# Optimization experiments

Hardware: AMD Instinct MI355X
Metric: run time of the kernel (lower is better)

The kernel has to match this reference:

```python
import jax, jax.numpy as jnp
import numpy as np
from jax import lax

M, N, Q = 256, 65536, 64
LAMBDA_STAR = 0.1
LAMBDA_O = 0.1
T_ITERS = 16
PM_ITERS = 100


def setup_inputs() -> dict:
    key = jax.random.key(0)
    kx, kd = jax.random.split(key)
    X = jax.random.normal(kx, (M, N), dtype=jnp.float32)
    D = jax.random.normal(kd, (M, Q), dtype=jnp.float32)
    return {"X": X, "D": D}


def _power_method(D):
    # Largest eigenvalue of D^T D via 100-step power iteration (fixed random init).
    x0 = jax.random.normal(jax.random.key(1), (1, Q), dtype=D.dtype)

    def step(x, _):
        x = (x @ D.T) @ D          # [1,q] -> [1,m] -> [1,q]
        nm = jnp.linalg.norm(x)
        return x / nm, nm

    _, nms = lax.scan(step, x0, None, length=PM_ITERS)
    return nms[-1]


def reference(X, D):
    m, n = X.shape
    q = D.shape[1]
    alpha = _power_method(D)
    eta = 1.0 / alpha

    Iq = jnp.eye(q, dtype=D.dtype)
    Im = jnp.eye(m, dtype=D.dtype)
    top = jnp.concatenate([D.T @ D + LAMBDA_STAR * Iq, D.T], axis=1)   # [q, q+m]
    bot = jnp.concatenate([D, (1.0 + LAMBDA_STAR) * Im], axis=1)       # [m, q+m]
    H = jnp.eye(m + q, dtype=D.dtype) - eta * jnp.concatenate([top, bot], axis=0)
    W = eta * jnp.concatenate([D.T, Im], axis=0)                        # [(m+q), m]
    t = LAMBDA_O * eta * jnp.concatenate([jnp.zeros(q, D.dtype), jnp.ones(m, D.dtype)])

    b0 = W @ X                                                           # [(m+q), n]
    Z0 = jnp.zeros((m + q, n), dtype=X.dtype)

    def ista_step(carry, _):
        Z, b = carry
        Znew = jnp.maximum(0.0, b - t[:, None])    # thresholding (ger(t, ones) == t broadcast)
        b = b + H @ (Znew - Z)
        return (Znew, b), None

    (Z, _), _ = lax.scan(ista_step, (Z0, b0), None, length=T_ITERS)
    return Z
```

## Files before the change

kernel.cpp:

```cpp
#include <hip/hip_runtime.h>


typedef __bf16 bf16x8 __attribute__((ext_vector_type(8)));
typedef __bf16 bf16x2 __attribute__((ext_vector_type(2)));
typedef float f32x4 __attribute__((ext_vector_type(4)));
typedef float f32x2 __attribute__((ext_vector_type(2)));

#define MFMA16(a, b, c) __builtin_amdgcn_mfma_f32_16x16x32_bf16((a), (b), (c), 0, 0, 0)

#define NTOT 65536
#define NCOL 16

__device__ __forceinline__ unsigned pk2(float a, float b) {
#if __has_builtin(__builtin_amdgcn_cvt_pk_bf16_f32)
  return __builtin_bit_cast(unsigned, __builtin_amdgcn_cvt_pk_bf16_f32(a, b));
#else
  unsigned short ua = __builtin_bit_cast(unsigned short, (__bf16)a);
  unsigned short ub = __builtin_bit_cast(unsigned short, (__bf16)b);
  return (unsigned)ua | ((unsigned)ub << 16);
#endif
}
__device__ __forceinline__ unsigned pk2v(f32x2 v) { return pk2(v[0], v[1]); }
__device__ __forceinline__ f32x2 f2(float s) { f32x2 v = {s, s}; return v; }
__device__ __forceinline__ f32x2 pfma(f32x2 a, f32x2 b, f32x2 c) {
  return __builtin_elementwise_fma(a, b, c);
}
__device__ __forceinline__ f32x2 pmax0(f32x2 a) {
  return __builtin_elementwise_max(a, f2(0.f));
}

#define GOF(row) ((row) * 68 + (((row) >> 3) << 2))
__global__ void rnmf_prep(const float* __restrict__ D, void* __restrict__ ws) {
  float* wsf = (float*)ws;
  __bf16* Dbf = (__bf16*)((char*)ws + 256);
  __bf16* DTbf = (__bf16*)((char*)ws + 256 + 32768);

  __shared__ __bf16 DTl[64 * 264];
  __shared__ __bf16 gA[64 * 72];
  __shared__ __bf16 gB[64 * 72];
  __shared__ float gf[64 * 68 + 32];
  __shared__ __align__(16) float xv[64];

  const int tid = threadIdx.x;
  const int w = tid >> 6, lane = tid & 63, c = lane & 15, q4 = lane >> 4;

#pragma unroll
  for (int e = 0; e < 16; ++e) {
    int i4 = e * 256 + tid;
    float4 dv = *(const float4*)(D + i4 * 4);
    uint2 u; u.x = pk2(dv.x, dv.y); u.y = pk2(dv.z, dv.w);
    *(uint2*)(Dbf + i4 * 4) = u;
  }
#pragma unroll
  for (int e = 0; e < 64; ++e) {
    int flat = e * 256 + tid;
    int k = flat >> 6, a = flat & 63;
    DTl[a * 264 + k] = (__bf16)D[k * 64 + a];
  }
  __syncthreads();
#pragma unroll
  for (int e = 0; e < 8; ++e) {
    int fi = e * 256 + tid;
    int a = fi >> 5;
    int k = (fi * 8) & 255;
    *(bf16x8*)(DTbf + fi * 8) = *(const bf16x8*)&DTl[a * 264 + k];
  }
#pragma unroll
  for (int ct = 0; ct < 4; ++ct) {
    f32x4 acc = {0.f, 0.f, 0.f, 0.f};
#pragma unroll
    for (int kb = 0; kb < 8; ++kb) {
      bf16x8 a = *(const bf16x8*)&DTl[(16 * w + c) * 264 + 32 * kb + 8 * q4];
      bf16x8 b = *(const bf16x8*)&DTl[(16 * ct + c) * 264 + 32 * kb + 8 * q4];
      acc = MFMA16(a, b, acc);
    }
#pragma unroll
    for (int r = 0; r < 4; ++r)
      gA[(16 * w + 4 * q4 + r) * 72 + 16 * ct + c] = (__bf16)acc[r];
  }
  __syncthreads();
#pragma unroll
  for (int ct = 0; ct < 4; ++ct) {
    f32x4 acc = {0.f, 0.f, 0.f, 0.f};
#pragma unroll
    for (int kb = 0; kb < 2; ++kb) {
      bf16x8 a = *(const bf16x8*)&gA[(16 * w + c) * 72 + 32 * kb + 8 * q4];
      bf16x8 b = *(const bf16x8*)&gA[(16 * ct + c) * 72 + 32 * kb + 8 * q4];
      acc = MFMA16(a, b, acc);
    }
#pragma unroll
    for (int r = 0; r < 4; ++r)
      gB[(16 * w + 4 * q4 + r) * 72 + 16 * ct + c] = (__bf16)acc[r];
  }
  __syncthreads();
#pragma unroll
  for (int ct = 0; ct < 4; ++ct) {
    f32x4 acc = {0.f, 0.f, 0.f, 0.f};
#pragma unroll
    for (int kb = 0; kb < 2; ++kb) {
      bf16x8 a = *(const bf16x8*)&gB[(16 * w + c) * 72 + 32 * kb + 8 * q4];
      bf16x8 b = *(const bf16x8*)&gB[(16 * ct + c) * 72 + 32 * kb + 8 * q4];
      acc = MFMA16(a, b, acc);
    }
#pragma unroll
    for (int r = 0; r < 4; ++r)
      gA[(16 * w + 4 * q4 + r) * 72 + 16 * ct + c] = (__bf16)acc[r];
  }
  __syncthreads();
#pragma unroll
  for (int ct = 0; ct < 4; ++ct) {
    f32x4 acc = {0.f, 0.f, 0.f, 0.f};
#pragma unroll
    for (int kb = 0; kb < 2; ++kb) {
      bf16x8 a = *(const bf16x8*)&gA[(16 * w + c) * 72 + 32 * kb + 8 * q4];
      bf16x8 b = *(const bf16x8*)&gA[(16 * ct + c) * 72 + 32 * kb + 8 * q4];
      acc = MFMA16(a, b, acc);
    }
#pragma unroll
    for (int r = 0; r < 4; ++r)
      gf[GOF(16 * w + 4 * q4 + r) + 16 * ct + c] = acc[r];
  }
  __syncthreads();

  if (w == 0) {
    float td = gf[GOF(lane) + lane];
#pragma unroll
    for (int off = 32; off; off >>= 1) td += __shfl_xor(td, off, 64);
    const float tr = td;
    const float itr = 1.f / tr;
    xv[lane] = 1.f;
    float nm = 1.f;
    const int rowoff = GOF(lane);
    for (int itp = 0; itp < 28; ++itp) {
      float a0 = 0.f, a1 = 0.f, a2 = 0.f, a3 = 0.f;
#pragma unroll
      for (int k = 0; k < 64; k += 16) {
        float4 ga = *(const float4*)&gf[rowoff + k];
        float4 xa = *(const float4*)&xv[k];
        float4 gb = *(const float4*)&gf[rowoff + k + 4];
        float4 xb = *(const float4*)&xv[k + 4];
        float4 gc = *(const float4*)&gf[rowoff + k + 8];
        float4 xc = *(const float4*)&xv[k + 8];
        float4 gd = *(const float4*)&gf[rowoff + k + 12];
        float4 xd = *(const float4*)&xv[k + 12];
        a0 = fmaf(ga.x, xa.x, a0); a0 = fmaf(ga.y, xa.y, a0);
        a0 = fmaf(ga.z, xa.z, a0); a0 = fmaf(ga.w, xa.w, a0);
        a1 = fmaf(gb.x, xb.x, a1); a1 = fmaf(gb.y, xb.y, a1);
        a1 = fmaf(gb.z, xb.z, a1); a1 = fmaf(gb.w, xb.w, a1);
        a2 = fmaf(gc.x, xc.x, a2); a2 = fmaf(gc.y, xc.y, a2);
        a2 = fmaf(gc.z, xc.z, a2); a2 = fmaf(gc.w, xc.w, a2);
        a3 = fmaf(gd.x, xd.x, a3); a3 = fmaf(gd.y, xd.y, a3);
        a3 = fmaf(gd.z, xd.z, a3); a3 = fmaf(gd.w, xd.w, a3);
      }
      float acc = (a0 + a1) + (a2 + a3);
      float y = acc * itr;
      float n2 = y * y;
#pragma unroll
      for (int off = 32; off; off >>= 1) n2 += __shfl_xor(n2, off, 64);
      nm = sqrtf(n2);
      xv[lane] = y / nm;
    }
    if (lane == 0) wsf[0] = 1.f / powf(nm * tr, 0.125f);
  }
}

__global__ __launch_bounds__(128, 2) void rnmf_main(const float* __restrict__ X,
                                                    float* __restrict__ Z,
                                                    const void* __restrict__ ws) {
  const float* wsf = (const float*)ws;
  const __bf16* Dbf = (const __bf16*)((const char*)ws + 256);
  const __bf16* DTbf = (const __bf16*)((const char*)ws + 256 + 32768);

  __shared__ __align__(16) char arena[16640];
  float* xs = (float*)arena;

  const int tid = threadIdx.x;
  const int w = tid >> 6;
  const int lane = tid & 63;
  const int c = lane & 15;
  const int q4 = lane >> 4;
  const int q4h = q4 >> 1, q4l = q4 & 1;
  const int wr = w;
  const int j0 = blockIdx.x * NCOL;

#pragma unroll
  for (int e = 0; e < 8; ++e) {
    int idx = e * 128 + tid;
    int row = idx >> 2, c4 = (idx & 3) * 4;
    float4 g = *(const float4*)(X + row * NTOT + j0 + c4);
    xs[(c4 + 0) * 260 + row] = g.x;
    xs[(c4 + 1) * 260 + row] = g.y;
    xs[(c4 + 2) * 260 + row] = g.z;
    xs[(c4 + 3) * 260 + row] = g.w;
  }

  const float eta = wsf[0];
  const f32x2 etav = f2(eta);
  const f32x2 metav = f2(-eta);
  const f32x2 cqv = f2(1.f - 0.1f * eta);
  const f32x2 cmv = f2(1.f - 1.1f * eta);
  const float tm = 0.1f * eta;

  bf16x8 d1[8][2];
#pragma unroll
  for (int rt = 0; rt < 8; ++rt)
#pragma unroll
    for (int kb = 0; kb < 2; ++kb)
      d1[rt][kb] = *(const bf16x8*)(Dbf + (128 * wr + 16 * rt + c) * 64 + 32 * kb + 8 * q4);
  bf16x8 d2[2][8];
#pragma unroll
  for (int rt2 = 0; rt2 < 2; ++rt2)
#pragma unroll
    for (int kb = 0; kb < 8; ++kb)
      d2[rt2][kb] = *(const bf16x8*)(DTbf + (32 * wr + 16 * rt2 + c) * 256 + 32 * kb + 8 * q4);

  __syncthreads();

  bf16x8 xb[8];
#pragma unroll
  for (int kb = 0; kb < 8; ++kb) {
    const float* p = &xs[c * 260 + 32 * kb + 8 * q4];
    float4 lo = *(const float4*)p;
    float4 hi = *(const float4*)(p + 4);
    uint4 packed = {pk2(lo.x, lo.y), pk2(lo.z, lo.w), pk2(hi.x, hi.y), pk2(hi.z, hi.w)};
    xb[kb] = __builtin_bit_cast(bf16x8, packed);
  }

  f32x2 bqt2[2][2];
#pragma unroll
  for (int rt2 = 0; rt2 < 2; ++rt2) {
    f32x4 acc = {0.f, 0.f, 0.f, 0.f};
#pragma unroll
    for (int kb = 0; kb < 8; ++kb) acc = MFMA16(d2[rt2][kb], xb[kb], acc);
    f32x2 a0 = {acc[0], acc[1]}, a1 = {acc[2], acc[3]};
    bqt2[rt2][0] = etav * a0;
    bqt2[rt2][1] = etav * a1;
  }

  f32x2 bmt2[8][2];
#pragma unroll
  for (int rt = 0; rt < 8; ++rt) {
    const float* p = &xs[c * 260 + 128 * wr + 16 * rt + 4 * q4];
    float4 v = *(const float4*)p;
    f32x2 x0 = {v.x, v.y}, x1 = {v.z, v.w};
    bmt2[rt][0] = pfma(etav, x0, f2(-tm));
    bmt2[rt][1] = pfma(etav, x1, f2(-tm));
  }

  __syncthreads();

  f32x2 zq2[2][2], zm2[8][2];
#pragma unroll
  for (int rt2 = 0; rt2 < 2; ++rt2)
#pragma unroll
    for (int p = 0; p < 2; ++p) zq2[rt2][p] = pmax0(bqt2[rt2][p]);
#pragma unroll
  for (int rt = 0; rt < 8; ++rt)
#pragma unroll
    for (int p = 0; p < 2; ++p) zm2[rt][p] = pmax0(bmt2[rt][p]);

  char* smem = arena;
  const int rb = lane * 16;
  const int zqrd = rb;
  const int vrd = 2048 + rb;
  const int wzq = wr * 1024 + q4h * 256 + c * 16 + 8 * q4l;
  const int wvb = 2048 + wr * 4096 + q4h * 256 + c * 16 + 8 * q4l;

#pragma unroll
  for (int rt2 = 0; rt2 < 2; ++rt2) {
    uint2 u; u.x = pk2v(zq2[rt2][0]); u.y = pk2v(zq2[rt2][1]);
    *(uint2*)(smem + wzq + rt2 * 512) = u;
  }

  for (int it = 0; it < 15; ++it) {
    __syncthreads();
    bf16x8 bz0 = *(const bf16x8*)(smem + zqrd);
    bf16x8 bz1 = *(const bf16x8*)(smem + zqrd + 1024);
#pragma unroll
    for (int rt = 0; rt < 8; ++rt) {
      f32x4 acc = {0.f, 0.f, 0.f, 0.f};
      acc = MFMA16(d1[rt][0], bz0, acc);
      acc = MFMA16(d1[rt][1], bz1, acc);
      f32x2 u0 = {acc[0], acc[1]}, u1 = {acc[2], acc[3]};
      f32x2 z0 = zm2[rt][0], z1v = zm2[rt][1];
      f32x2 v0 = u0 + z0, v1 = u1 + z1v;
      f32x2 t0 = pfma(cmv, z0, bmt2[rt][0]);
      f32x2 t1 = pfma(cmv, z1v, bmt2[rt][1]);
      zm2[rt][0] = pmax0(pfma(metav, u0, t0));
      zm2[rt][1] = pmax0(pfma(metav, u1, t1));
      uint2 uu; uu.x = pk2v(v0); uu.y = pk2v(v1);
      *(uint2*)(smem + wvb + rt * 512) = uu;
    }
    __syncthreads();
    f32x4 aA0 = {0.f, 0.f, 0.f, 0.f}, aA1 = {0.f, 0.f, 0.f, 0.f};
    f32x4 aB0 = {0.f, 0.f, 0.f, 0.f}, aB1 = {0.f, 0.f, 0.f, 0.f};
#pragma unroll
    for (int kb = 0; kb < 4; ++kb) {
      bf16x8 bv = *(const bf16x8*)(smem + vrd + kb * 1024);
      aA0 = MFMA16(d2[0][kb], bv, aA0);
      aA1 = MFMA16(d2[1][kb], bv, aA1);
    }
#pragma unroll
    for (int kb = 4; kb < 8; ++kb) {
      bf16x8 bv = *(const bf16x8*)(smem + vrd + kb * 1024);
      aB0 = MFMA16(d2[0][kb], bv, aB0);
      aB1 = MFMA16(d2[1][kb], bv, aB1);
    }
    f32x4 s0 = aA0 + aB0;
    f32x4 s1 = aA1 + aB1;
    {
      f32x2 w0 = {s0[0], s0[1]}, w1 = {s0[2], s0[3]};
      f32x2 t0 = pfma(cqv, zq2[0][0], bqt2[0][0]);
      f32x2 t1 = pfma(cqv, zq2[0][1], bqt2[0][1]);
      zq2[0][0] = pmax0(pfma(metav, w0, t0));
      zq2[0][1] = pmax0(pfma(metav, w1, t1));
      uint2 u; u.x = pk2v(zq2[0][0]); u.y = pk2v(zq2[0][1]);
      *(uint2*)(smem + wzq) = u;
    }
    {
      f32x2 w0 = {s1[0], s1[1]}, w1 = {s1[2], s1[3]};
      f32x2 t0 = pfma(cqv, zq2[1][0], bqt2[1][0]);
      f32x2 t1 = pfma(cqv, zq2[1][1], bqt2[1][1]);
      zq2[1][0] = pmax0(pfma(metav, w0, t0));
      zq2[1][1] = pmax0(pfma(metav, w1, t1));
      uint2 u; u.x = pk2v(zq2[1][0]); u.y = pk2v(zq2[1][1]);
      *(uint2*)(smem + wzq + 512) = u;
    }
  }

#pragma unroll
  for (int rt2 = 0; rt2 < 2; ++rt2)
#pragma unroll
    for (int p = 0; p < 2; ++p)
#pragma unroll
      for (int e = 0; e < 2; ++e)
        Z[(32 * wr + 16 * rt2 + 4 * q4 + 2 * p + e) * NTOT + j0 + c] = zq2[rt2][p][e];
#pragma unroll
  for (int rt = 0; rt < 8; ++rt)
#pragma unroll
    for (int p = 0; p < 2; ++p)
#pragma unroll
      for (int e = 0; e < 2; ++e)
        Z[(64 + 128 * wr + 16 * rt + 4 * q4 + 2 * p + e) * NTOT + j0 + c] = zm2[rt][p][e];
}

extern "C" void kernel_launch(void* const* d_in, const int* in_sizes, int n_in,
                              void* d_out, int out_size, void* d_ws, size_t ws_size,
                              hipStream_t stream) {
  const float* X = (const float*)d_in[0];
  const float* D = (const float*)d_in[1];
  float* Z = (float*)d_out;
  rnmf_prep<<<dim3(1), dim3(256), 0, stream>>>(D, d_ws);
  rnmf_main<<<dim3(NTOT / NCOL), dim3(128), 0, stream>>>(X, Z, d_ws);
}
```

Measured before the change: 235.8 us.

## Use precomputed D^T D and double-buffered LDS to halve barriers per ISTA iteration

Stores the bf16 Gram matrix D^T D from the prep kernel to workspace. The main kernel computes the q-row update as G·zq plus D^T·zm directly, replacing the old chained D^T(D·zq + zm) product. With this, both halves of the update read only the previous iterate, so each iteration needs one barrier instead of two; LDS is double-buffered (ping-pong offsets) to keep this safe. In exchange it adds four small MFMAs per iteration, extra registers for the Gram fragments, more shared memory per block, and a different bf16 rounding path.

```diff
diff --git a/kernel.cpp b/kernel.cpp
--- a/kernel.cpp
+++ b/kernel.cpp
@@ -2,7 +2,6 @@
 
 
 typedef __bf16 bf16x8 __attribute__((ext_vector_type(8)));
-typedef __bf16 bf16x2 __attribute__((ext_vector_type(2)));
 typedef float f32x4 __attribute__((ext_vector_type(4)));
 typedef float f32x2 __attribute__((ext_vector_type(2)));
 
@@ -34,6 +33,7 @@
   float* wsf = (float*)ws;
   __bf16* Dbf = (__bf16*)((char*)ws + 256);
   __bf16* DTbf = (__bf16*)((char*)ws + 256 + 32768);
+  __bf16* Gbf = (__bf16*)((char*)ws + 256 + 65536);
 
   __shared__ __bf16 DTl[64 * 264];
   __shared__ __bf16 gA[64 * 72];
@@ -75,8 +75,11 @@
       acc = MFMA16(a, b, acc);
     }
 #pragma unroll
-    for (int r = 0; r < 4; ++r)
-      gA[(16 * w + 4 * q4 + r) * 72 + 16 * ct + c] = (__bf16)acc[r];
+    for (int r = 0; r < 4; ++r) {
+      __bf16 gb = (__bf16)acc[r];
+      gA[(16 * w + 4 * q4 + r) * 72 + 16 * ct + c] = gb;
+      Gbf[(16 * w + 4 * q4 + r) * 64 + 16 * ct + c] = gb;
+    }
   }
   __syncthreads();
 #pragma unroll
@@ -170,9 +173,11 @@
   const float* wsf = (const float*)ws;
   const __bf16* Dbf = (const __bf16*)((const char*)ws + 256);
   const __bf16* DTbf = (const __bf16*)((const char*)ws + 256 + 32768);
-
-  __shared__ __align__(16) char arena[16640];
+  const __bf16* Gbf = (const __bf16*)((const char*)ws + 256 + 65536);
+
+  __shared__ __align__(16) char arena[20480];
   float* xs = (float*)arena;
+  char* smem = arena;
 
   const int tid = threadIdx.x;
   const int w = tid >> 6;
@@ -180,7 +185,6 @@
   const int c = lane & 15;
   const int q4 = lane >> 4;
   const int q4h = q4 >> 1, q4l = q4 & 1;
-  const int wr = w;
   const int j0 = blockIdx.x * NCOL;
 
 #pragma unroll
@@ -206,13 +210,19 @@
   for (int rt = 0; rt < 8; ++rt)
 #pragma unroll
     for (int kb = 0; kb < 2; ++kb)
-      d1[rt][kb] = *(const bf16x8*)(Dbf + (128 * wr + 16 * rt + c) * 64 + 32 * kb + 8 * q4);
+      d1[rt][kb] = *(const bf16x8*)(Dbf + (128 * w + 16 * rt + c) * 64 + 32 * kb + 8 * q4);
   bf16x8 d2[2][8];
 #pragma unroll
   for (int rt2 = 0; rt2 < 2; ++rt2)
 #pragma unroll
     for (int kb = 0; kb < 8; ++kb)
-      d2[rt2][kb] = *(const bf16x8*)(DTbf + (32 * wr + 16 * rt2 + c) * 256 + 32 * kb + 8 * q4);
+      d2[rt2][kb] = *(const bf16x8*)(DTbf + (32 * w + 16 * rt2 + c) * 256 + 32 * kb + 8 * q4);
+  bf16x8 gq[2][2];
+#pragma unroll
+  for (int rt2 = 0; rt2 < 2; ++rt2)
+#pragma unroll
+    for (int kb = 0; kb < 2; ++kb)
+      gq[rt2][kb] = *(const bf16x8*)(Gbf + (32 * w + 16 * rt2 + c) * 64 + 32 * kb + 8 * q4);
 
   __syncthreads();
 
@@ -240,7 +250,7 @@
   f32x2 bmt2[8][2];
 #pragma unroll
   for (int rt = 0; rt < 8; ++rt) {
-    const float* p = &xs[c * 260 + 128 * wr + 16 * rt + 4 * q4];
+    const float* p = &xs[c * 260 + 128 * w + 16 * rt + 4 * q4];
     float4 v = *(const float4*)p;
     f32x2 x0 = {v.x, v.y}, x1 = {v.z, v.w};
     bmt2[rt][0] = pfma(etav, x0, f2(-tm));
@@ -259,55 +269,49 @@
 #pragma unroll
     for (int p = 0; p < 2; ++p) zm2[rt][p] = pmax0(bmt2[rt][p]);
 
-  char* smem = arena;
   const int rb = lane * 16;
-  const int zqrd = rb;
-  const int vrd = 2048 + rb;
-  const int wzq = wr * 1024 + q4h * 256 + c * 16 + 8 * q4l;
-  const int wvb = 2048 + wr * 4096 + q4h * 256 + c * 16 + 8 * q4l;
+  const int wzq = w * 1024 + q4h * 256 + c * 16 + 8 * q4l;
+  const int wzm = 2048 + w * 4096 + q4h * 256 + c * 16 + 8 * q4l;
 
 #pragma unroll
   for (int rt2 = 0; rt2 < 2; ++rt2) {
     uint2 u; u.x = pk2v(zq2[rt2][0]); u.y = pk2v(zq2[rt2][1]);
     *(uint2*)(smem + wzq + rt2 * 512) = u;
   }
-
-  for (int it = 0; it < 15; ++it) {
+#pragma unroll
+  for (int rt = 0; rt < 8; ++rt) {
+    uint2 u; u.x = pk2v(zm2[rt][0]); u.y = pk2v(zm2[rt][1]);
+    *(uint2*)(smem + wzm + rt * 512) = u;
+  }
+
+  auto ITER = [&](const int cb, const int nb) {
     __syncthreads();
-    bf16x8 bz0 = *(const bf16x8*)(smem + zqrd);
-    bf16x8 bz1 = *(const bf16x8*)(smem + zqrd + 1024);
+    bf16x8 zqf0 = *(const bf16x8*)(smem + cb + rb);
+    bf16x8 zqf1 = *(const bf16x8*)(smem + cb + 1024 + rb);
+    f32x4 s0 = {0.f, 0.f, 0.f, 0.f}, s1 = {0.f, 0.f, 0.f, 0.f};
+    s0 = MFMA16(gq[0][0], zqf0, s0);
+    s0 = MFMA16(gq[0][1], zqf1, s0);
+    s1 = MFMA16(gq[1][0], zqf0, s1);
+    s1 = MFMA16(gq[1][1], zqf1, s1);
 #pragma unroll
     for (int rt = 0; rt < 8; ++rt) {
       f32x4 acc = {0.f, 0.f, 0.f, 0.f};
-      acc = MFMA16(d1[rt][0], bz0, acc);
-      acc = MFMA16(d1[rt][1], bz1, acc);
+      acc = MFMA16(d1[rt][0], zqf0, acc);
+      acc = MFMA16(d1[rt][1], zqf1, acc);
       f32x2 u0 = {acc[0], acc[1]}, u1 = {acc[2], acc[3]};
-      f32x2 z0 = zm2[rt][0], z1v = zm2[rt][1];
-      f32x2 v0 = u0 + z0, v1 = u1 + z1v;
-      f32x2 t0 = pfma(cmv, z0, bmt2[rt][0]);
-      f32x2 t1 = pfma(cmv, z1v, bmt2[rt][1]);
+      f32x2 t0 = pfma(cmv, zm2[rt][0], bmt2[rt][0]);
+      f32x2 t1 = pfma(cmv, zm2[rt][1], bmt2[rt][1]);
       zm2[rt][0] = pmax0(pfma(metav, u0, t0));
       zm2[rt][1] = pmax0(pfma(metav, u1, t1));
-      uint2 uu; uu.x = pk2v(v0); uu.y = pk2v(v1);
-      *(uint2*)(smem + wvb + rt * 512) = uu;
-    }
-    __syncthreads();
-    f32x4 aA0 = {0.f, 0.f, 0.f, 0.f}, aA1 = {0.f, 0.f, 0.f, 0.f};
-    f32x4 aB0 = {0.f, 0.f, 0.f, 0.f}, aB1 = {0.f, 0.f, 0.f, 0.f};
-#pragma unroll
-    for (int kb = 0; kb < 4; ++kb) {
-      bf16x8 bv = *(const bf16x8*)(smem + vrd + kb * 1024);
-      aA0 = MFMA16(d2[0][kb], bv, aA0);
-      aA1 = MFMA16(d2[1][kb], bv, aA1);
-    }
-#pragma unroll
-    for (int kb = 4; kb < 8; ++kb) {
-      bf16x8 bv = *(const bf16x8*)(smem + vrd + kb * 1024);
-      aB0 = MFMA16(d2[0][kb], bv, aB0);
-      aB1 = MFMA16(d2[1][kb], bv, aB1);
-    }
-    f32x4 s0 = aA0 + aB0;
-    f32x4 s1 = aA1 + aB1;
+      uint2 uu; uu.x = pk2v(zm2[rt][0]); uu.y = pk2v(zm2[rt][1]);
+      *(uint2*)(smem + nb + wzm + rt * 512) = uu;
+    }
+#pragma unroll
+    for (int kb = 0; kb < 8; ++kb) {
+      bf16x8 zmf = *(const bf16x8*)(smem + cb + 2048 + kb * 1024 + rb);
+      s0 = MFMA16(d2[0][kb], zmf, s0);
+      s1 = MFMA16(d2[1][kb], zmf, s1);
+    }
     {
       f32x2 w0 = {s0[0], s0[1]}, w1 = {s0[2], s0[3]};
       f32x2 t0 = pfma(cqv, zq2[0][0], bqt2[0][0]);
@@ -315,7 +319,7 @@
       zq2[0][0] = pmax0(pfma(metav, w0, t0));
       zq2[0][1] = pmax0(pfma(metav, w1, t1));
       uint2 u; u.x = pk2v(zq2[0][0]); u.y = pk2v(zq2[0][1]);
-      *(uint2*)(smem + wzq) = u;
+      *(uint2*)(smem + nb + wzq) = u;
     }
     {
       f32x2 w0 = {s1[0], s1[1]}, w1 = {s1[2], s1[3]};
@@ -324,9 +328,16 @@
       zq2[1][0] = pmax0(pfma(metav, w0, t0));
       zq2[1][1] = pmax0(pfma(metav, w1, t1));
       uint2 u; u.x = pk2v(zq2[1][0]); u.y = pk2v(zq2[1][1]);
-      *(uint2*)(smem + wzq + 512) = u;
-    }
-  }
+      *(uint2*)(smem + nb + wzq + 512) = u;
+    }
+  };
+
+#pragma unroll 1
+  for (int it2 = 0; it2 < 7; ++it2) {
+    ITER(0, 10240);
+    ITER(10240, 0);
+  }
+  ITER(0, 10240);
 
 #pragma unroll
   for (int rt2 = 0; rt2 < 2; ++rt2)
@@ -334,14 +345,14 @@
     for (int p = 0; p < 2; ++p)
 #pragma unroll
       for (int e = 0; e < 2; ++e)
-        Z[(32 * wr + 16 * rt2 + 4 * q4 + 2 * p + e) * NTOT + j0 + c] = zq2[rt2][p][e];
+        Z[(32 * w + 16 * rt2 + 4 * q4 + 2 * p + e) * NTOT + j0 + c] = zq2[rt2][p][e];
 #pragma unroll
   for (int rt = 0; rt < 8; ++rt)
 #pragma unroll
     for (int p = 0; p < 2; ++p)
 #pragma unroll
       for (int e = 0; e < 2; ++e)
-        Z[(64 + 128 * wr + 16 * rt + 4 * q4 + 2 * p + e) * NTOT + j0 + c] = zm2[rt][p][e];
+        Z[(64 + 128 * w + 16 * rt + 4 * q4 + 2 * p + e) * NTOT + j0 + c] = zm2[rt][p][e];
 }
 
 extern "C" void kernel_launch(void* const* d_in, const int* in_sizes, int n_in,
```

After: 239.1 us. About the same (+1.4%).
